# Optimization experiments

Measured on AMD Instinct MI355X. Metric: run time of the kernel, lower is better.

## Reference

```python
import jax, jax.numpy as jnp
import numpy as np

N_NODES = 50000
N_EDGES = 800000
N_GRAPHS = 64
ALPHA = 0.5
LN_EPS = 1e-5


def _gcn(x, W, b, src, dst, n):
    """GCNConv: h = D^{-1/2}(A+I)D^{-1/2} (x W) + b, edges already include self-loops."""
    h = x @ W                                             # [N, F]
    ones = jnp.ones(src.shape[0], dtype=h.dtype)
    deg = jax.ops.segment_sum(ones, dst, num_segments=n)  # in-degree (target side)
    dinv = jnp.where(deg > 0, jax.lax.rsqrt(deg), 0.0)
    norm = dinv[src] * dinv[dst]                          # [E]
    msg = h[src] * norm[:, None]                          # gather + scale
    return jax.ops.segment_sum(msg, dst, num_segments=n) + b


def _dirgnn(x, W_in, b_in, W_out, b_out, src, dst, n):
    # conv_in on original edges, conv_out on flipped edges; root_weight=False
    x_in = _gcn(x, W_in, b_in, src, dst, n)
    x_out = _gcn(x, W_out, b_out, dst, src, n)
    return ALPHA * x_out + (1.0 - ALPHA) * x_in


def setup_inputs() -> dict:
    key = jax.random.key(0)
    ks = jax.random.split(key, 16)
    d = {}
    d["x"] = jax.random.normal(ks[0], (N_NODES, 64), jnp.float32)
    d["edge_src"] = jax.random.randint(ks[1], (N_EDGES,), 0, N_NODES, jnp.int32)
    d["edge_dst"] = jax.random.randint(ks[2], (N_EDGES,), 0, N_NODES, jnp.int32)
    d["batch"] = jnp.sort(jax.random.randint(ks[3], (N_NODES,), 0, N_GRAPHS, jnp.int32))
    s = 1.0 / np.sqrt(64.0)
    for i, nm in enumerate(["W1_in", "W1_out", "W2_in", "W2_out", "W3_in", "W3_out"]):
        d[nm] = jax.random.normal(ks[4 + i], (64, 64), jnp.float32) * s
        d[nm.replace("W", "b")] = jnp.zeros((64,), jnp.float32)
    d["ln_w"] = jnp.ones((64,), jnp.float32)
    d["ln_b"] = jnp.zeros((64,), jnp.float32)
    d["P1_w"] = jax.random.normal(ks[10], (64, 128), jnp.float32) * s
    d["P1_b"] = jnp.zeros((128,), jnp.float32)
    d["P2_w"] = jax.random.normal(ks[11], (128, 2), jnp.float32) * (1.0 / np.sqrt(128.0))
    d["P2_b"] = jnp.zeros((2,), jnp.float32)
    return d


def reference(x, edge_src, edge_dst, batch,
              W1_in, b1_in, W1_out, b1_out,
              W2_in, b2_in, W2_out, b2_out,
              W3_in, b3_in, W3_out, b3_out,
              ln_w, ln_b, P1_w, P1_b, P2_w, P2_b):
    n = x.shape[0]
    ar = jnp.arange(n, dtype=edge_src.dtype)
    src = jnp.concatenate([edge_src, ar])   # add self-loops once
    dst = jnp.concatenate([edge_dst, ar])

    h = _dirgnn(x, W1_in, b1_in, W1_out, b1_out, src, dst, n)
    h = jax.nn.relu(h)
    h = _dirgnn(h, W2_in, b2_in, W2_out, b2_out, src, dst, n)
    h = jax.nn.relu(h)   # dropout p=0 in eval
    h = _dirgnn(h, W3_in, b3_in, W3_out, b3_out, src, dst, n)

    # global_mean_pool over graphs
    sums = jax.ops.segment_sum(h, batch, num_segments=N_GRAPHS)
    cnt = jax.ops.segment_sum(jnp.ones((n,), h.dtype), batch, num_segments=N_GRAPHS)
    pooled = sums / jnp.maximum(cnt, 1.0)[:, None]        # [G, 64]

    # LayerNorm
    mu = jnp.mean(pooled, axis=-1, keepdims=True)
    var = jnp.mean(jnp.square(pooled - mu), axis=-1, keepdims=True)
    z = (pooled - mu) * jax.lax.rsqrt(var + LN_EPS) * ln_w + ln_b

    z = jax.nn.relu(z @ P1_w + P1_b)
    return z @ P2_w + P2_b                                 # [G, 2]
```

## Files before the change

### kernel.cpp

```cpp
#include <hip/hip_runtime.h>

#define N_NODES 50000
#define N_EDGES 800000
#define N_GRAPHS 64
#define LN_EPS 1e-5f
#define NPAD 50176


__global__ __launch_bounds__(256) void init_kernel(int* deg_in, int* deg_out,
                                                   int* gc, float* pool_sum, int* cnt) {
    int i = blockIdx.x * 256 + threadIdx.x;
    if (i < N_NODES) { deg_in[i] = 1; deg_out[i] = 1; }
    if (i < 2) gc[i] = 0;
    if (i < N_GRAPHS * 64) pool_sum[i] = 0.f;
    if (i < N_GRAPHS) cnt[i] = 0;
}

__global__ __launch_bounds__(256) void degree_kernel(const int* __restrict__ src,
                                                     const int* __restrict__ dst,
                                                     int* deg_in, int* deg_out) {
    int e = blockIdx.x * 256 + threadIdx.x;
    if (e >= N_EDGES) return;
    atomicAdd(&deg_in[dst[e]], 1);
    atomicAdd(&deg_out[src[e]], 1);
}

__global__ __launch_bounds__(256) void prep_kernel(
    const int* __restrict__ deg_in, const int* __restrict__ deg_out,
    float* __restrict__ dinv_in, float* __restrict__ dinv_out,
    int* __restrict__ base_in, int* __restrict__ base_out,
    int* __restrict__ cur_in, int* __restrict__ cur_out, int* gc) {
    __shared__ int lws[4];
    const int i = blockIdx.x * 256 + threadIdx.x;
    const int tid = threadIdx.x, lane = tid & 63, wid = tid >> 6;

#pragma unroll
    for (int dir = 0; dir < 2; ++dir) {
        const int* deg = dir ? deg_out : deg_in;
        float* dinv    = dir ? dinv_out : dinv_in;
        int* base      = dir ? base_out : base_in;
        int* cur       = dir ? cur_out : cur_in;
        int d = (i < N_NODES) ? deg[i] : 1;
        if (i < N_NODES) dinv[i] = rsqrtf((float)d);
        int v = d - 1;
        int s = v;
#pragma unroll
        for (int off = 1; off < 64; off <<= 1) {
            int t = __shfl_up(s, off);
            if (lane >= off) s += t;
        }
        if (lane == 63) lws[wid] = s;
        __syncthreads();
        if (tid == 0) {
            int tmp[4]; int tot = 0;
            for (int w = 0; w < 4; ++w) { tmp[w] = tot; tot += lws[w]; }
            int bb = atomicAdd(&gc[dir], tot);
            for (int w = 0; w < 4; ++w) lws[w] = bb + tmp[w];
        }
        __syncthreads();
        int b = lws[wid] + s - v;
        if (i < N_NODES) { base[i] = b; cur[i] = b; }
        __syncthreads();
    }
}

__global__ __launch_bounds__(256) void scatter_kernel(
    const int* __restrict__ src, const int* __restrict__ dst,
    int* cur_in, int* cur_out, int* __restrict__ csr_in, int* __restrict__ csr_out) {
    int e = blockIdx.x * 256 + threadIdx.x;
    if (e >= N_EDGES) return;
    int s = src[e], d = dst[e];
    int p = atomicAdd(&cur_in[d], 1);
    csr_in[p] = s;
    int q = atomicAdd(&cur_out[s], 1);
    csr_out[q] = d;
}

__global__ __launch_bounds__(256) void aggregate_kernel(
    const float* __restrict__ act,
    const int* __restrict__ deg_in, const int* __restrict__ deg_out,
    const float* __restrict__ dinv_in, const float* __restrict__ dinv_out,
    const int* __restrict__ base_in, const int* __restrict__ base_out,
    const int* __restrict__ csr_in, const int* __restrict__ csr_out,
    float* __restrict__ AggIn, float* __restrict__ AggOut) {
    int node = (blockIdx.x << 2) + (threadIdx.x >> 6);
    if (node >= N_NODES) return;
    const int lane = threadIdx.x & 63;
    const float di = dinv_in[node];
    const float dq = dinv_out[node];
    const float self = act[(size_t)node * 64 + lane];
    float aI = self * di * di;
    float aO = self * dq * dq;
    {
        const int b = base_in[node];
        const int n = deg_in[node] - 1;
        int j = 0;
        for (; j + 4 <= n; j += 4) {
            int s0 = __builtin_amdgcn_readfirstlane(csr_in[b + j]);
            int s1 = __builtin_amdgcn_readfirstlane(csr_in[b + j + 1]);
            int s2 = __builtin_amdgcn_readfirstlane(csr_in[b + j + 2]);
            int s3 = __builtin_amdgcn_readfirstlane(csr_in[b + j + 3]);
            float w0 = dinv_in[s0], w1 = dinv_in[s1];
            float w2 = dinv_in[s2], w3 = dinv_in[s3];
            float v0 = act[(size_t)s0 * 64 + lane];
            float v1 = act[(size_t)s1 * 64 + lane];
            float v2 = act[(size_t)s2 * 64 + lane];
            float v3 = act[(size_t)s3 * 64 + lane];
            aI += di * (w0 * v0 + w1 * v1 + w2 * v2 + w3 * v3);
        }
        for (; j < n; ++j) {
            int s0 = __builtin_amdgcn_readfirstlane(csr_in[b + j]);
            aI += di * dinv_in[s0] * act[(size_t)s0 * 64 + lane];
        }
    }
    {
        const int b = base_out[node];
        const int n = deg_out[node] - 1;
        int j = 0;
        for (; j + 4 <= n; j += 4) {
            int s0 = __builtin_amdgcn_readfirstlane(csr_out[b + j]);
            int s1 = __builtin_amdgcn_readfirstlane(csr_out[b + j + 1]);
            int s2 = __builtin_amdgcn_readfirstlane(csr_out[b + j + 2]);
            int s3 = __builtin_amdgcn_readfirstlane(csr_out[b + j + 3]);
            float w0 = dinv_out[s0], w1 = dinv_out[s1];
            float w2 = dinv_out[s2], w3 = dinv_out[s3];
            float v0 = act[(size_t)s0 * 64 + lane];
            float v1 = act[(size_t)s1 * 64 + lane];
            float v2 = act[(size_t)s2 * 64 + lane];
            float v3 = act[(size_t)s3 * 64 + lane];
            aO += dq * (w0 * v0 + w1 * v1 + w2 * v2 + w3 * v3);
        }
        for (; j < n; ++j) {
            int s0 = __builtin_amdgcn_readfirstlane(csr_out[b + j]);
            aO += dq * dinv_out[s0] * act[(size_t)s0 * 64 + lane];
        }
    }
    AggIn[(size_t)node * 64 + lane]  = aI;
    AggOut[(size_t)node * 64 + lane] = aO;
}

__global__ __launch_bounds__(256) void gemm_combine_kernel(
    const float* __restrict__ Ain, const float* __restrict__ Aout,
    const float* __restrict__ Win, const float* __restrict__ Wout,
    const float* __restrict__ b_in, const float* __restrict__ b_out,
    float* __restrict__ act, int do_relu) {
    __shared__ __align__(16) float sWin[64 * 64];
    __shared__ __align__(16) float sWout[64 * 64];
    __shared__ __align__(16) float sAin[64 * 68];
    __shared__ __align__(16) float sAout[64 * 68];
    const int tx = threadIdx.x;
    for (int i = tx * 4; i < 4096; i += 1024) {
        *(float4*)&sWin[i]  = *(const float4*)&Win[i];
        *(float4*)&sWout[i] = *(const float4*)&Wout[i];
    }
    const int row0 = blockIdx.x * 64;
    for (int i = tx; i < 1024; i += 256) {
        int r = i >> 4;
        int k4 = (i & 15) << 2;
        int gr = row0 + r;
        float4 vi = make_float4(0.f, 0.f, 0.f, 0.f);
        float4 vo = vi;
        if (gr < N_NODES) {
            vi = *(const float4*)&Ain[(size_t)gr * 64 + k4];
            vo = *(const float4*)&Aout[(size_t)gr * 64 + k4];
        }
        *(float4*)&sAin[r * 68 + k4]  = vi;
        *(float4*)&sAout[r * 68 + k4] = vo;
    }
    __syncthreads();
    const int ct = tx & 15;
    const int rg = tx >> 4;
    const int c4 = ct << 2;
    float aI[4][4], aO[4][4];
#pragma unroll
    for (int i = 0; i < 4; ++i)
#pragma unroll
        for (int j = 0; j < 4; ++j) { aI[i][j] = 0.f; aO[i][j] = 0.f; }
#pragma unroll 4
    for (int k0 = 0; k0 < 64; k0 += 4) {
        float4 avI[4], avO[4];
#pragma unroll
        for (int i = 0; i < 4; ++i) {
            avI[i] = *(float4*)&sAin[(rg * 4 + i) * 68 + k0];
            avO[i] = *(float4*)&sAout[(rg * 4 + i) * 68 + k0];
        }
#pragma unroll
        for (int kk = 0; kk < 4; ++kk) {
            float4 wi = *(float4*)&sWin[(k0 + kk) * 64 + c4];
            float4 wo = *(float4*)&sWout[(k0 + kk) * 64 + c4];
#pragma unroll
            for (int i = 0; i < 4; ++i) {
                float ai = (&avI[i].x)[kk];
                float ao = (&avO[i].x)[kk];
                aI[i][0] += ai * wi.x; aI[i][1] += ai * wi.y;
                aI[i][2] += ai * wi.z; aI[i][3] += ai * wi.w;
                aO[i][0] += ao * wo.x; aO[i][1] += ao * wo.y;
                aO[i][2] += ao * wo.z; aO[i][3] += ao * wo.w;
            }
        }
    }
    float4 bi = *(const float4*)&b_in[c4];
    float4 bo = *(const float4*)&b_out[c4];
#pragma unroll
    for (int i = 0; i < 4; ++i) {
        int gr = row0 + rg * 4 + i;
        if (gr < N_NODES) {
            float4 r;
            r.x = 0.5f * (aO[i][0] + bo.x) + 0.5f * (aI[i][0] + bi.x);
            r.y = 0.5f * (aO[i][1] + bo.y) + 0.5f * (aI[i][1] + bi.y);
            r.z = 0.5f * (aO[i][2] + bo.z) + 0.5f * (aI[i][2] + bi.z);
            r.w = 0.5f * (aO[i][3] + bo.w) + 0.5f * (aI[i][3] + bi.w);
            if (do_relu) {
                r.x = fmaxf(r.x, 0.f); r.y = fmaxf(r.y, 0.f);
                r.z = fmaxf(r.z, 0.f); r.w = fmaxf(r.w, 0.f);
            }
            *(float4*)&act[(size_t)gr * 64 + c4] = r;
        }
    }
}

__global__ __launch_bounds__(256) void pool_kernel(
    const float* __restrict__ h, const int* __restrict__ batch,
    float* __restrict__ pool_sum, int* __restrict__ cnt) {
    int w = (blockIdx.x << 2) + (threadIdx.x >> 6);
    int n0 = w << 5;
    if (n0 >= N_NODES) return;
    const int lane = threadIdx.x & 63;
    int n1 = min(n0 + 32, N_NODES);
    int g = batch[n0];
    float acc = 0.f;
    int run = 0;
    for (int nn = n0; nn < n1; ++nn) {
        int bg = batch[nn];
        if (bg != g) {
            unsafeAtomicAdd(&pool_sum[g * 64 + lane], acc);
            if (lane == 0) atomicAdd(&cnt[g], run);
            acc = 0.f; run = 0; g = bg;
        }
        acc += h[(size_t)nn * 64 + lane];
        run++;
    }
    unsafeAtomicAdd(&pool_sum[g * 64 + lane], acc);
    if (lane == 0) atomicAdd(&cnt[g], run);
}

__global__ __launch_bounds__(64) void head_kernel(
    const float* __restrict__ pool_sum, const int* __restrict__ cnt,
    const float* __restrict__ ln_w, const float* __restrict__ ln_b,
    const float* __restrict__ P1w, const float* __restrict__ P1b,
    const float* __restrict__ P2w, const float* __restrict__ P2b,
    float* __restrict__ out) {
    __shared__ float zbuf[64];
    const int g = blockIdx.x, f = threadIdx.x;
    float c = fmaxf((float)cnt[g], 1.0f);
    float p = pool_sum[g * 64 + f] / c;
    float s = p;
#pragma unroll
    for (int o = 32; o >= 1; o >>= 1) s += __shfl_xor(s, o);
    float mu = s * (1.0f / 64.0f);
    float dv = p - mu;
    float q = dv * dv;
#pragma unroll
    for (int o = 32; o >= 1; o >>= 1) q += __shfl_xor(q, o);
    float var = q * (1.0f / 64.0f);
    float z = dv * rsqrtf(var + LN_EPS) * ln_w[f] + ln_b[f];
    zbuf[f] = z;
    __syncthreads();
    float s0 = 0.f, s1 = 0.f;
#pragma unroll 8
    for (int k = 0; k < 64; ++k) {
        float zk = zbuf[k];
        s0 += zk * P1w[k * 128 + f];
        s1 += zk * P1w[k * 128 + f + 64];
    }
    float r0 = fmaxf(s0 + P1b[f], 0.f);
    float r1 = fmaxf(s1 + P1b[f + 64], 0.f);
    float p0 = r0 * P2w[f * 2 + 0] + r1 * P2w[(f + 64) * 2 + 0];
    float p1 = r0 * P2w[f * 2 + 1] + r1 * P2w[(f + 64) * 2 + 1];
#pragma unroll
    for (int o = 32; o >= 1; o >>= 1) {
        p0 += __shfl_xor(p0, o);
        p1 += __shfl_xor(p1, o);
    }
    if (f == 0) {
        out[g * 2 + 0] = p0 + P2b[0];
        out[g * 2 + 1] = p1 + P2b[1];
    }
}

extern "C" void kernel_launch(void* const* d_in, const int* in_sizes, int n_in,
                              void* d_out, int out_size, void* d_ws, size_t ws_size,
                              hipStream_t stream) {
    const float* x     = (const float*)d_in[0];
    const int* esrc    = (const int*)d_in[1];
    const int* edst    = (const int*)d_in[2];
    const int* batch   = (const int*)d_in[3];
    const float* W1_in  = (const float*)d_in[4];
    const float* b1_in  = (const float*)d_in[5];
    const float* W1_out = (const float*)d_in[6];
    const float* b1_out = (const float*)d_in[7];
    const float* W2_in  = (const float*)d_in[8];
    const float* b2_in  = (const float*)d_in[9];
    const float* W2_out = (const float*)d_in[10];
    const float* b2_out = (const float*)d_in[11];
    const float* W3_in  = (const float*)d_in[12];
    const float* b3_in  = (const float*)d_in[13];
    const float* W3_out = (const float*)d_in[14];
    const float* b3_out = (const float*)d_in[15];
    const float* ln_w  = (const float*)d_in[16];
    const float* ln_b  = (const float*)d_in[17];
    const float* P1w   = (const float*)d_in[18];
    const float* P1b   = (const float*)d_in[19];
    const float* P2w   = (const float*)d_in[20];
    const float* P2b   = (const float*)d_in[21];
    float* out = (float*)d_out;

    float* ws = (float*)d_ws;
    const size_t NF = (size_t)N_NODES * 64;
    int*   deg_in   = (int*)(ws + 0 * NPAD);
    int*   deg_out  = (int*)(ws + 1 * NPAD);
    float* dinv_in  = ws + 2 * NPAD;
    float* dinv_out = ws + 3 * NPAD;
    int*   base_in  = (int*)(ws + 4 * NPAD);
    int*   base_out = (int*)(ws + 5 * NPAD);
    int*   cur_in   = (int*)(ws + 6 * NPAD);
    int*   cur_out  = (int*)(ws + 7 * NPAD);
    int*   gc       = (int*)(ws + 8 * NPAD);
    float* pool_sum = ws + 8 * NPAD + 64;
    int*   cnt      = (int*)(ws + 8 * NPAD + 64 + 4096);
    float* act      = ws + 9 * NPAD;
    float* AggIn    = act + NF;
    float* AggOut   = AggIn + NF;
    int*   csr_in   = (int*)(AggOut + NF);
    int*   csr_out  = csr_in + N_EDGES;

    const int nblk = (N_NODES + 255) / 256;
    init_kernel<<<nblk, 256, 0, stream>>>(deg_in, deg_out, gc, pool_sum, cnt);
    degree_kernel<<<(N_EDGES + 255) / 256, 256, 0, stream>>>(esrc, edst, deg_in, deg_out);
    prep_kernel<<<nblk, 256, 0, stream>>>(deg_in, deg_out, dinv_in, dinv_out,
                                          base_in, base_out, cur_in, cur_out, gc);
    scatter_kernel<<<(N_EDGES + 255) / 256, 256, 0, stream>>>(esrc, edst, cur_in, cur_out,
                                                              csr_in, csr_out);

    const int agg_grid  = (N_NODES + 3) / 4;
    const int gemm_grid = (N_NODES + 63) / 64;

    aggregate_kernel<<<agg_grid, 256, 0, stream>>>(x, deg_in, deg_out, dinv_in, dinv_out,
                                                   base_in, base_out, csr_in, csr_out,
                                                   AggIn, AggOut);
    gemm_combine_kernel<<<gemm_grid, 256, 0, stream>>>(AggIn, AggOut, W1_in, W1_out,
                                                       b1_in, b1_out, act, 1);
    aggregate_kernel<<<agg_grid, 256, 0, stream>>>(act, deg_in, deg_out, dinv_in, dinv_out,
                                                   base_in, base_out, csr_in, csr_out,
                                                   AggIn, AggOut);
    gemm_combine_kernel<<<gemm_grid, 256, 0, stream>>>(AggIn, AggOut, W2_in, W2_out,
                                                       b2_in, b2_out, act, 1);
    aggregate_kernel<<<agg_grid, 256, 0, stream>>>(act, deg_in, deg_out, dinv_in, dinv_out,
                                                   base_in, base_out, csr_in, csr_out,
                                                   AggIn, AggOut);
    gemm_combine_kernel<<<gemm_grid, 256, 0, stream>>>(AggIn, AggOut, W3_in, W3_out,
                                                       b3_in, b3_out, act, 0);

    pool_kernel<<<(N_NODES + 127) / 128, 256, 0, stream>>>(act, batch, pool_sum, cnt);
    head_kernel<<<N_GRAPHS, 64, 0, stream>>>(pool_sum, cnt, ln_w, ln_b, P1w, P1b, P2w, P2b, out);
}
```

Before: 585.8 us.

## Partition degree and CSR build atomics by XCD node range; unroll aggregation by 8

The degree and scatter kernels now launch 8x128 blocks. Each group of blocks, selected by blockIdx mod 8 and assumed to map to one XCD, scans all edges but only does atomics on nodes in its own slice of the node range. This is meant to keep atomic traffic local to one L2 instead of spreading it across dies, at the cost of every group reading the full edge list. The aggregation loop is also unrolled from 4 to 8 gathers for more memory-level parallelism, and the normalisation multiply is moved out of the loop.

```diff
diff --git a/kernel.cpp b/kernel.cpp
--- a/kernel.cpp
+++ b/kernel.cpp
@@ -5,6 +5,9 @@
 #define N_GRAPHS 64
 #define LN_EPS 1e-5f
 #define NPAD 50176
+#define NXCD 8
+#define NODES_PER_GRP (N_NODES / NXCD)
+#define BPG 128
 
 
 __global__ __launch_bounds__(256) void init_kernel(int* deg_in, int* deg_out,
@@ -19,10 +22,14 @@
 __global__ __launch_bounds__(256) void degree_kernel(const int* __restrict__ src,
                                                      const int* __restrict__ dst,
                                                      int* deg_in, int* deg_out) {
-    int e = blockIdx.x * 256 + threadIdx.x;
-    if (e >= N_EDGES) return;
-    atomicAdd(&deg_in[dst[e]], 1);
-    atomicAdd(&deg_out[src[e]], 1);
+    const int g   = blockIdx.x & (NXCD - 1);
+    const int sub = blockIdx.x >> 3;
+    const int lo = g * NODES_PER_GRP, hi = lo + NODES_PER_GRP;
+    for (int e = sub * 256 + threadIdx.x; e < N_EDGES; e += BPG * 256) {
+        int s = src[e], d = dst[e];
+        if (d >= lo && d < hi) atomicAdd(&deg_in[d], 1);
+        if (s >= lo && s < hi) atomicAdd(&deg_out[s], 1);
+    }
 }
 
 __global__ __launch_bounds__(256) void prep_kernel(
@@ -64,16 +71,24 @@
     }
 }
 
-__global__ __launch_bounds__(256) void scatter_kernel(
+
+__global__ __launch_bounds__(256) void place_kernel(
     const int* __restrict__ src, const int* __restrict__ dst,
     int* cur_in, int* cur_out, int* __restrict__ csr_in, int* __restrict__ csr_out) {
-    int e = blockIdx.x * 256 + threadIdx.x;
-    if (e >= N_EDGES) return;
-    int s = src[e], d = dst[e];
-    int p = atomicAdd(&cur_in[d], 1);
-    csr_in[p] = s;
-    int q = atomicAdd(&cur_out[s], 1);
-    csr_out[q] = d;
+    const int g   = blockIdx.x & (NXCD - 1);
+    const int sub = blockIdx.x >> 3;
+    const int lo = g * NODES_PER_GRP, hi = lo + NODES_PER_GRP;
+    for (int e = sub * 256 + threadIdx.x; e < N_EDGES; e += BPG * 256) {
+        int s = src[e], d = dst[e];
+        if (d >= lo && d < hi) {
+            int p = atomicAdd(&cur_in[d], 1);
+            csr_in[p] = s;
+        }
+        if (s >= lo && s < hi) {
+            int q = atomicAdd(&cur_out[s], 1);
+            csr_out[q] = d;
+        }
+    }
 }
 
 __global__ __launch_bounds__(256) void aggregate_kernel(
@@ -89,54 +104,71 @@
     const float di = dinv_in[node];
     const float dq = dinv_out[node];
     const float self = act[(size_t)node * 64 + lane];
-    float aI = self * di * di;
-    float aO = self * dq * dq;
+    float sumI = 0.f, sumO = 0.f;
     {
         const int b = base_in[node];
         const int n = deg_in[node] - 1;
         int j = 0;
-        for (; j + 4 <= n; j += 4) {
+        for (; j + 8 <= n; j += 8) {
             int s0 = __builtin_amdgcn_readfirstlane(csr_in[b + j]);
             int s1 = __builtin_amdgcn_readfirstlane(csr_in[b + j + 1]);
             int s2 = __builtin_amdgcn_readfirstlane(csr_in[b + j + 2]);
             int s3 = __builtin_amdgcn_readfirstlane(csr_in[b + j + 3]);
-            float w0 = dinv_in[s0], w1 = dinv_in[s1];
-            float w2 = dinv_in[s2], w3 = dinv_in[s3];
+            int s4 = __builtin_amdgcn_readfirstlane(csr_in[b + j + 4]);
+            int s5 = __builtin_amdgcn_readfirstlane(csr_in[b + j + 5]);
+            int s6 = __builtin_amdgcn_readfirstlane(csr_in[b + j + 6]);
+            int s7 = __builtin_amdgcn_readfirstlane(csr_in[b + j + 7]);
+            float w0 = dinv_in[s0], w1 = dinv_in[s1], w2 = dinv_in[s2], w3 = dinv_in[s3];
+            float w4 = dinv_in[s4], w5 = dinv_in[s5], w6 = dinv_in[s6], w7 = dinv_in[s7];
             float v0 = act[(size_t)s0 * 64 + lane];
             float v1 = act[(size_t)s1 * 64 + lane];
             float v2 = act[(size_t)s2 * 64 + lane];
             float v3 = act[(size_t)s3 * 64 + lane];
-            aI += di * (w0 * v0 + w1 * v1 + w2 * v2 + w3 * v3);
+            float v4 = act[(size_t)s4 * 64 + lane];
+            float v5 = act[(size_t)s5 * 64 + lane];
+            float v6 = act[(size_t)s6 * 64 + lane];
+            float v7 = act[(size_t)s7 * 64 + lane];
+            sumI += (w0 * v0 + w1 * v1 + w2 * v2 + w3 * v3)
+                  + (w4 * v4 + w5 * v5 + w6 * v6 + w7 * v7);
         }
         for (; j < n; ++j) {
             int s0 = __builtin_amdgcn_readfirstlane(csr_in[b + j]);
-            aI += di * dinv_in[s0] * act[(size_t)s0 * 64 + lane];
+            sumI += dinv_in[s0] * act[(size_t)s0 * 64 + lane];
         }
     }
     {
         const int b = base_out[node];
         const int n = deg_out[node] - 1;
         int j = 0;
-        for (; j + 4 <= n; j += 4) {
+        for (; j + 8 <= n; j += 8) {
             int s0 = __builtin_amdgcn_readfirstlane(csr_out[b + j]);
             int s1 = __builtin_amdgcn_readfirstlane(csr_out[b + j + 1]);
             int s2 = __builtin_amdgcn_readfirstlane(csr_out[b + j + 2]);
             int s3 = __builtin_amdgcn_readfirstlane(csr_out[b + j + 3]);
-            float w0 = dinv_out[s0], w1 = dinv_out[s1];
-            float w2 = dinv_out[s2], w3 = dinv_out[s3];
+            int s4 = __builtin_amdgcn_readfirstlane(csr_out[b + j + 4]);
+            int s5 = __builtin_amdgcn_readfirstlane(csr_out[b + j + 5]);
+            int s6 = __builtin_amdgcn_readfirstlane(csr_out[b + j + 6]);
+            int s7 = __builtin_amdgcn_readfirstlane(csr_out[b + j + 7]);
+            float w0 = dinv_out[s0], w1 = dinv_out[s1], w2 = dinv_out[s2], w3 = dinv_out[s3];
+            float w4 = dinv_out[s4], w5 = dinv_out[s5], w6 = dinv_out[s6], w7 = dinv_out[s7];
             float v0 = act[(size_t)s0 * 64 + lane];
             float v1 = act[(size_t)s1 * 64 + lane];
             float v2 = act[(size_t)s2 * 64 + lane];
             float v3 = act[(size_t)s3 * 64 + lane];
-            aO += dq * (w0 * v0 + w1 * v1 + w2 * v2 + w3 * v3);
+            float v4 = act[(size_t)s4 * 64 + lane];
+            float v5 = act[(size_t)s5 * 64 + lane];
+            float v6 = act[(size_t)s6 * 64 + lane];
+            float v7 = act[(size_t)s7 * 64 + lane];
+            sumO += (w0 * v0 + w1 * v1 + w2 * v2 + w3 * v3)
+                  + (w4 * v4 + w5 * v5 + w6 * v6 + w7 * v7);
         }
         for (; j < n; ++j) {
             int s0 = __builtin_amdgcn_readfirstlane(csr_out[b + j]);
-            aO += dq * dinv_out[s0] * act[(size_t)s0 * 64 + lane];
-        }
-    }
-    AggIn[(size_t)node * 64 + lane]  = aI;
-    AggOut[(size_t)node * 64 + lane] = aO;
+            sumO += dinv_out[s0] * act[(size_t)s0 * 64 + lane];
+        }
+    }
+    AggIn[(size_t)node * 64 + lane]  = di * (di * self + sumI);
+    AggOut[(size_t)node * 64 + lane] = dq * (dq * self + sumO);
 }
 
 __global__ __launch_bounds__(256) void gemm_combine_kernel(
@@ -336,11 +368,11 @@
 
     const int nblk = (N_NODES + 255) / 256;
     init_kernel<<<nblk, 256, 0, stream>>>(deg_in, deg_out, gc, pool_sum, cnt);
-    degree_kernel<<<(N_EDGES + 255) / 256, 256, 0, stream>>>(esrc, edst, deg_in, deg_out);
+    degree_kernel<<<NXCD * BPG, 256, 0, stream>>>(esrc, edst, deg_in, deg_out);
     prep_kernel<<<nblk, 256, 0, stream>>>(deg_in, deg_out, dinv_in, dinv_out,
                                           base_in, base_out, cur_in, cur_out, gc);
-    scatter_kernel<<<(N_EDGES + 255) / 256, 256, 0, stream>>>(esrc, edst, cur_in, cur_out,
-                                                              csr_in, csr_out);
+    place_kernel<<<NXCD * BPG, 256, 0, stream>>>(esrc, edst, cur_in, cur_out,
+                                                 csr_in, csr_out);
 
     const int agg_grid  = (N_NODES + 3) / 4;
     const int gemm_grid = (N_NODES + 63) / 64;
```

Measured after the change: 538.5 us. -8.1%, faster.
